# Optimization experiments

Hardware: AMD Instinct MI355X
Metric: run time of the kernel (lower is better)

## Reference

```python
import jax, jax.numpy as jnp
import numpy as np

ORIENTATIONS = 8
CELL = 16          # pixels_per_cell = (16, 16)
EPS = 1e-5         # skimage L2-Hys eps


def _hog_features(x):
    """x: [B, H, W, C] float image. Faithful to skimage.feature.hog with
    orientations=8, pixels_per_cell=(16,16), cells_per_block=(1,1),
    block_norm='L2-Hys', multichannel gradient selection."""
    B, H, W, C = x.shape
    # per-channel central-difference gradients, zero at borders (skimage _hog_channel_gradient)
    g_row = jnp.zeros_like(x).at[:, 1:-1, :, :].set(x[:, 2:, :, :] - x[:, :-2, :, :])
    g_col = jnp.zeros_like(x).at[:, :, 1:-1, :].set(x[:, :, 2:, :] - x[:, :, :-2, :])
    magn_ch = jnp.hypot(g_row, g_col)                      # [B,H,W,C]
    # pick channel with max gradient magnitude per pixel
    idx = jnp.argmax(magn_ch, axis=-1, keepdims=True)      # [B,H,W,1]
    gr = jnp.take_along_axis(g_row, idx, axis=-1)[..., 0]  # [B,H,W]
    gc = jnp.take_along_axis(g_col, idx, axis=-1)[..., 0]
    magn = jnp.take_along_axis(magn_ch, idx, axis=-1)[..., 0]
    # orientation in degrees, mod 180 (unsigned gradients)
    ori = jnp.degrees(jnp.arctan2(gr, gc)) % 180.0
    bin_width = 180.0 / ORIENTATIONS
    bin_idx = jnp.clip(jnp.floor(ori / bin_width).astype(jnp.int32), 0, ORIENTATIONS - 1)
    ncr, ncc = H // CELL, W // CELL
    # per-cell mean magnitude for each orientation bin
    hists = []
    for o in range(ORIENTATIONS):
        m = jnp.where(bin_idx == o, magn, 0.0)             # [B,H,W]
        m = m.reshape(B, ncr, CELL, ncc, CELL).mean(axis=(2, 4))  # [B,ncr,ncc]
        hists.append(m)
    hist = jnp.stack(hists, axis=-1)                       # [B,ncr,ncc,O]
    # block normalization: 1x1 cells per block, 'L2-Hys'
    n = hist / jnp.sqrt(jnp.sum(hist * hist, axis=-1, keepdims=True) + EPS ** 2)
    n = jnp.minimum(n, 0.2)
    n = n / jnp.sqrt(jnp.sum(n * n, axis=-1, keepdims=True) + EPS ** 2)
    return n.reshape(B, -1)                                # [B, ncr*ncc*O]


def setup_inputs() -> dict:
    key = jax.random.key(0)
    fake = jax.random.uniform(key, (64, 3, 512, 512), dtype=jnp.float32)
    return {"fake": fake}


def reference(fake) -> jnp.ndarray:
    x = jnp.transpose(fake, (0, 2, 3, 1))  # NCHW -> NHWC (module's permute)
    return _hog_features(x)
```

## Files before the change

### kernel.cpp

```cpp
#include <hip/hip_runtime.h>
#include <math.h>


namespace {

constexpr int Hh = 512;
constexpr int Ww = 512;
constexpr int CHN = 3;
constexpr int HW = Hh * Ww;
constexpr float TAN22 = 0.41421356237309503f;

__device__ __forceinline__ void load_row4(const float* __restrict__ xb,
                                          int h, int c0, int lane,
                                          float dst[CHN][4]) {
    const int hl = h < 0 ? 0 : (h > Hh - 1 ? Hh - 1 : h);
#pragma unroll
    for (int ch = 0; ch < CHN; ++ch) {
        const float4 v = *(const float4*)(xb + (size_t)ch * HW +
                                          (size_t)hl * Ww + c0 + (lane << 2));
        dst[ch][0] = v.x; dst[ch][1] = v.y; dst[ch][2] = v.z; dst[ch][3] = v.w;
    }
}

__global__ __launch_bounds__(256) void hog_kernel(const float* __restrict__ x,
                                                  float* __restrict__ out) {
    const int b       = blockIdx.x >> 5;
    const int cellrow = blockIdx.x & 31;
    const int tx      = threadIdx.x;
    const int lane    = tx & 63;
    const int wid     = tx >> 6;
    const int colhalf = wid & 1;
    const int strip   = wid >> 1;
    const int r0      = cellrow * 16 + strip * 8;
    const int c0      = colhalf << 8;

    const float* xb = x + (size_t)b * (CHN * HW);

    const bool bL = (colhalf == 0) & (lane == 0);
    const bool bR = (colhalf == 1) & (lane == 63);
    const int hLoff = (colhalf == 0) ? 0 : 255;
    const int hRoff = (colhalf == 0) ? 256 : 511;

    float P[CHN][4], C[CHN][4], N[CHN][4], T[CHN][4];
    load_row4(xb, r0 - 1, c0, lane, P);
    load_row4(xb, r0,     c0, lane, C);
    load_row4(xb, r0 + 1, c0, lane, N);

    float hLc[CHN], hRc[CHN], hLn[CHN], hRn[CHN];
#pragma unroll
    for (int ch = 0; ch < CHN; ++ch) {
        const float* rp = xb + (size_t)ch * HW + (size_t)r0 * Ww;
        hLc[ch] = rp[hLoff];
        hRc[ch] = rp[hRoff];
    }

    float c[8];
#pragma unroll
    for (int o = 0; o < 8; ++o) c[o] = 0.f;

#pragma unroll 1
    for (int hh = 0; hh < 8; ++hh) {
        const int h = r0 + hh;

        if (hh < 7) load_row4(xb, h + 2, c0, lane, T);
        {
            const int hn = (h + 1 > Hh - 1) ? Hh - 1 : h + 1;
#pragma unroll
            for (int ch = 0; ch < CHN; ++ch) {
                const float* rp = xb + (size_t)ch * HW + (size_t)hn * Ww;
                hLn[ch] = rp[hLoff];
                hRn[ch] = rp[hRoff];
            }
        }

        const bool rowEdge = (h == 0) | (h == Hh - 1);

        float gL[CHN], gR[CHN];
#pragma unroll
        for (int ch = 0; ch < CHN; ++ch) {
            const float su = __shfl_up(C[ch][3], 1, 64);
            const float sd = __shfl_down(C[ch][0], 1, 64);
            gL[ch] = (lane == 0)  ? hLc[ch] : su;
            gR[ch] = (lane == 63) ? hRc[ch] : sd;
        }

#pragma unroll
        for (int i = 0; i < 4; ++i) {
            float bm2 = -1.f, bgr = 0.f, bgc = 0.f;
#pragma unroll
            for (int ch = 0; ch < CHN; ++ch) {
                const float gl  = (i == 0) ? gL[ch] : C[ch][i - 1];
                const float gr_ = (i == 3) ? gR[ch] : C[ch][i + 1];
                float gcol = gr_ - gl;
                if (i == 0) gcol = bL ? 0.f : gcol;
                if (i == 3) gcol = bR ? 0.f : gcol;
                float gv = N[ch][i] - P[ch][i];
                gv = rowEdge ? 0.f : gv;
                const float m2 = fmaf(gv, gv, gcol * gcol);
                if (m2 > bm2) { bm2 = m2; bgr = gv; bgc = gcol; }
            }
            const float m = sqrtf(bm2);

            const bool flip = (bgr < 0.f) | ((bgr == 0.f) & (bgc < 0.f));
            const float bb = flip ? -bgr : bgr;
            const float A  = flip ? -bgc : bgc;
            const float Aa = fabsf(A);
            const float p1 = Aa * TAN22;
            const float p2 = bb * TAN22;
            const bool q2  = (A <= 0.f);
            const bool ge1 = (bb >= p1), ge2 = (bb >= Aa), ge3 = (p2 >= Aa);
            const bool gt1 = (bb > p1),  gt2 = (bb > Aa),  gt3 = (p2 > Aa);
            c[0] += m;
            c[1] += (q2 | ge1) ? m : 0.f;
            c[2] += (q2 | ge2) ? m : 0.f;
            c[3] += (q2 | ge3) ? m : 0.f;
            c[4] += q2 ? m : 0.f;
            c[5] += (q2 & !gt3) ? m : 0.f;
            c[6] += (q2 & !gt2) ? m : 0.f;
            c[7] += (q2 & !gt1) ? m : 0.f;
        }

        if (hh < 7) {
#pragma unroll
            for (int ch = 0; ch < CHN; ++ch) {
#pragma unroll
                for (int i = 0; i < 4; ++i) {
                    P[ch][i] = C[ch][i];
                    C[ch][i] = N[ch][i];
                    N[ch][i] = T[ch][i];
                }
                hLc[ch] = hLn[ch];
                hRc[ch] = hRn[ch];
            }
        }
    }

#pragma unroll
    for (int o = 0; o < 8; ++o) {
        c[o] += __shfl_xor(c[o], 1, 64);
        c[o] += __shfl_xor(c[o], 2, 64);
    }

    __shared__ float lh[2][32][9];
    if (tx < 64) lh[tx >> 5][tx & 31][8] = 0.f;
    if ((lane & 3) == 0) {
        const int cell = (colhalf << 4) + (lane >> 2);
#pragma unroll
        for (int o = 0; o < 8; ++o) lh[strip][cell][o] = c[o];
    }
    __syncthreads();

    const int cell = tx >> 3;
    const int o    = tx & 7;
    const float c_o  = lh[0][cell][o]     + lh[1][cell][o];
    const float c_o1 = lh[0][cell][o + 1] + lh[1][cell][o + 1];
    const float hv = (c_o - c_o1) * (1.0f / 256.0f);

    float ss = hv * hv;
    ss += __shfl_xor(ss, 1, 64);
    ss += __shfl_xor(ss, 2, 64);
    ss += __shfl_xor(ss, 4, 64);
    float n1 = hv / sqrtf(ss + 1e-10f);
    n1 = fminf(n1, 0.2f);
    float s2 = n1 * n1;
    s2 += __shfl_xor(s2, 1, 64);
    s2 += __shfl_xor(s2, 2, 64);
    s2 += __shfl_xor(s2, 4, 64);
    const float nv = n1 / sqrtf(s2 + 1e-10f);

    out[(((size_t)b * 32 + cellrow) * 32 + cell) * 8 + o] = nv;
}

}

extern "C" void kernel_launch(void* const* d_in, const int* in_sizes, int n_in,
                              void* d_out, int out_size, void* d_ws, size_t ws_size,
                              hipStream_t stream) {
    (void)n_in; (void)out_size; (void)d_ws; (void)ws_size;
    const float* x = (const float*)d_in[0];
    float* out = (float*)d_out;
    const int B = in_sizes[0] / (CHN * HW);
    const int grid = B * 32;
    hog_kernel<<<grid, 256, 0, stream>>>(x, out);
}
```

Measured before the change: 282.9 us.

## Split blocks by column half and preload all strip rows up front

Each block now covers one column half of a cell row, which doubles the grid. Each wave handles a 4-row strip instead of 8, and all six needed rows are loaded into registers before any compute starts. This replaces the rolling per-row prefetch loop, so more memory loads are in flight at once and latency is easier to hide. The horizontal halo values are fetched once per wave and handed out with shuffles instead of per-row scalar loads. In exchange, more halo rows are re-read (6 loads for 4 output rows rather than 10 for 8), register use goes up (launch bounds 256,4), and half the threads sit idle in the final normalization.

```diff
diff --git a/kernel.cpp b/kernel.cpp
--- a/kernel.cpp
+++ b/kernel.cpp
@@ -10,78 +10,59 @@
 constexpr int HW = Hh * Ww;
 constexpr float TAN22 = 0.41421356237309503f;
 
-__device__ __forceinline__ void load_row4(const float* __restrict__ xb,
-                                          int h, int c0, int lane,
-                                          float dst[CHN][4]) {
-    const int hl = h < 0 ? 0 : (h > Hh - 1 ? Hh - 1 : h);
-#pragma unroll
-    for (int ch = 0; ch < CHN; ++ch) {
-        const float4 v = *(const float4*)(xb + (size_t)ch * HW +
-                                          (size_t)hl * Ww + c0 + (lane << 2));
-        dst[ch][0] = v.x; dst[ch][1] = v.y; dst[ch][2] = v.z; dst[ch][3] = v.w;
-    }
-}
-
-__global__ __launch_bounds__(256) void hog_kernel(const float* __restrict__ x,
-                                                  float* __restrict__ out) {
-    const int b       = blockIdx.x >> 5;
-    const int cellrow = blockIdx.x & 31;
+__global__ __launch_bounds__(256, 4) void hog_kernel(const float* __restrict__ x,
+                                                     float* __restrict__ out) {
+    const int b       = blockIdx.x >> 6;
+    const int cellrow = (blockIdx.x >> 1) & 31;
+    const int colhalf = blockIdx.x & 1;
     const int tx      = threadIdx.x;
     const int lane    = tx & 63;
     const int wid     = tx >> 6;
-    const int colhalf = wid & 1;
-    const int strip   = wid >> 1;
-    const int r0      = cellrow * 16 + strip * 8;
+    const int r0      = cellrow * 16 + wid * 4;
     const int c0      = colhalf << 8;
 
     const float* xb = x + (size_t)b * (CHN * HW);
 
+    float4 R[6][CHN];
+#pragma unroll
+    for (int r = 0; r < 6; ++r) {
+        int h = r0 - 1 + r;
+        h = h < 0 ? 0 : (h > Hh - 1 ? Hh - 1 : h);
+#pragma unroll
+        for (int ch = 0; ch < CHN; ++ch)
+            R[r][ch] = *(const float4*)(xb + (size_t)ch * HW +
+                                        (size_t)h * Ww + c0 + (lane << 2));
+    }
+
+    float halov = 0.f;
+    if (lane < 24) {
+        const int ch = lane >> 3, r = (lane >> 1) & 3, side = lane & 1;
+        int wcol = side ? c0 + 256 : c0 - 1;
+        wcol = wcol < 0 ? 0 : (wcol > Ww - 1 ? Ww - 1 : wcol);
+        halov = xb[(size_t)ch * HW + (size_t)(r0 + r) * Ww + wcol];
+    }
+
     const bool bL = (colhalf == 0) & (lane == 0);
     const bool bR = (colhalf == 1) & (lane == 63);
-    const int hLoff = (colhalf == 0) ? 0 : 255;
-    const int hRoff = (colhalf == 0) ? 256 : 511;
-
-    float P[CHN][4], C[CHN][4], N[CHN][4], T[CHN][4];
-    load_row4(xb, r0 - 1, c0, lane, P);
-    load_row4(xb, r0,     c0, lane, C);
-    load_row4(xb, r0 + 1, c0, lane, N);
-
-    float hLc[CHN], hRc[CHN], hLn[CHN], hRn[CHN];
-#pragma unroll
-    for (int ch = 0; ch < CHN; ++ch) {
-        const float* rp = xb + (size_t)ch * HW + (size_t)r0 * Ww;
-        hLc[ch] = rp[hLoff];
-        hRc[ch] = rp[hRoff];
-    }
 
     float c[8];
 #pragma unroll
     for (int o = 0; o < 8; ++o) c[o] = 0.f;
 
-#pragma unroll 1
-    for (int hh = 0; hh < 8; ++hh) {
+#pragma unroll
+    for (int hh = 0; hh < 4; ++hh) {
         const int h = r0 + hh;
-
-        if (hh < 7) load_row4(xb, h + 2, c0, lane, T);
-        {
-            const int hn = (h + 1 > Hh - 1) ? Hh - 1 : h + 1;
-#pragma unroll
-            for (int ch = 0; ch < CHN; ++ch) {
-                const float* rp = xb + (size_t)ch * HW + (size_t)hn * Ww;
-                hLn[ch] = rp[hLoff];
-                hRn[ch] = rp[hRoff];
-            }
-        }
-
         const bool rowEdge = (h == 0) | (h == Hh - 1);
 
         float gL[CHN], gR[CHN];
 #pragma unroll
         for (int ch = 0; ch < CHN; ++ch) {
-            const float su = __shfl_up(C[ch][3], 1, 64);
-            const float sd = __shfl_down(C[ch][0], 1, 64);
-            gL[ch] = (lane == 0)  ? hLc[ch] : su;
-            gR[ch] = (lane == 63) ? hRc[ch] : sd;
+            const float su = __shfl_up(R[hh + 1][ch].w, 1, 64);
+            const float sd = __shfl_down(R[hh + 1][ch].x, 1, 64);
+            const float hl = __shfl(halov, (ch << 3) | (hh << 1), 64);
+            const float hr = __shfl(halov, (ch << 3) | (hh << 1) | 1, 64);
+            gL[ch] = (lane == 0)  ? hl : su;
+            gR[ch] = (lane == 63) ? hr : sd;
         }
 
 #pragma unroll
@@ -89,12 +70,18 @@
             float bm2 = -1.f, bgr = 0.f, bgc = 0.f;
 #pragma unroll
             for (int ch = 0; ch < CHN; ++ch) {
-                const float gl  = (i == 0) ? gL[ch] : C[ch][i - 1];
-                const float gr_ = (i == 3) ? gR[ch] : C[ch][i + 1];
+                const float4 pv = R[hh][ch];
+                const float4 cv = R[hh + 1][ch];
+                const float4 nv = R[hh + 2][ch];
+                const float pr_[4] = {pv.x, pv.y, pv.z, pv.w};
+                const float cu_[4] = {cv.x, cv.y, cv.z, cv.w};
+                const float nx_[4] = {nv.x, nv.y, nv.z, nv.w};
+                const float gl  = (i == 0) ? gL[ch] : cu_[i - 1];
+                const float gr_ = (i == 3) ? gR[ch] : cu_[i + 1];
                 float gcol = gr_ - gl;
                 if (i == 0) gcol = bL ? 0.f : gcol;
                 if (i == 3) gcol = bR ? 0.f : gcol;
-                float gv = N[ch][i] - P[ch][i];
+                float gv = nx_[i] - pr_[i];
                 gv = rowEdge ? 0.f : gv;
                 const float m2 = fmaf(gv, gv, gcol * gcol);
                 if (m2 > bm2) { bm2 = m2; bgr = gv; bgc = gcol; }
@@ -119,20 +106,6 @@
             c[6] += (q2 & !gt2) ? m : 0.f;
             c[7] += (q2 & !gt1) ? m : 0.f;
         }
-
-        if (hh < 7) {
-#pragma unroll
-            for (int ch = 0; ch < CHN; ++ch) {
-#pragma unroll
-                for (int i = 0; i < 4; ++i) {
-                    P[ch][i] = C[ch][i];
-                    C[ch][i] = N[ch][i];
-                    N[ch][i] = T[ch][i];
-                }
-                hLc[ch] = hLn[ch];
-                hRc[ch] = hRn[ch];
-            }
-        }
     }
 
 #pragma unroll
@@ -141,34 +114,38 @@
         c[o] += __shfl_xor(c[o], 2, 64);
     }
 
-    __shared__ float lh[2][32][9];
-    if (tx < 64) lh[tx >> 5][tx & 31][8] = 0.f;
+    __shared__ float lh[4][16][9];
+    if (tx < 64) lh[tx >> 4][tx & 15][8] = 0.f;
     if ((lane & 3) == 0) {
-        const int cell = (colhalf << 4) + (lane >> 2);
+        const int cell = lane >> 2;
 #pragma unroll
-        for (int o = 0; o < 8; ++o) lh[strip][cell][o] = c[o];
+        for (int o = 0; o < 8; ++o) lh[wid][cell][o] = c[o];
     }
     __syncthreads();
 
-    const int cell = tx >> 3;
-    const int o    = tx & 7;
-    const float c_o  = lh[0][cell][o]     + lh[1][cell][o];
-    const float c_o1 = lh[0][cell][o + 1] + lh[1][cell][o + 1];
-    const float hv = (c_o - c_o1) * (1.0f / 256.0f);
+    if (tx < 128) {
+        const int cell = tx >> 3;
+        const int o    = tx & 7;
+        const float c_o  = lh[0][cell][o]     + lh[1][cell][o] +
+                           lh[2][cell][o]     + lh[3][cell][o];
+        const float c_o1 = lh[0][cell][o + 1] + lh[1][cell][o + 1] +
+                           lh[2][cell][o + 1] + lh[3][cell][o + 1];
+        const float hv = (c_o - c_o1) * (1.0f / 256.0f);
 
-    float ss = hv * hv;
-    ss += __shfl_xor(ss, 1, 64);
-    ss += __shfl_xor(ss, 2, 64);
-    ss += __shfl_xor(ss, 4, 64);
-    float n1 = hv / sqrtf(ss + 1e-10f);
-    n1 = fminf(n1, 0.2f);
-    float s2 = n1 * n1;
-    s2 += __shfl_xor(s2, 1, 64);
-    s2 += __shfl_xor(s2, 2, 64);
-    s2 += __shfl_xor(s2, 4, 64);
-    const float nv = n1 / sqrtf(s2 + 1e-10f);
+        float ss = hv * hv;
+        ss += __shfl_xor(ss, 1, 64);
+        ss += __shfl_xor(ss, 2, 64);
+        ss += __shfl_xor(ss, 4, 64);
+        float n1 = hv / sqrtf(ss + 1e-10f);
+        n1 = fminf(n1, 0.2f);
+        float s2 = n1 * n1;
+        s2 += __shfl_xor(s2, 1, 64);
+        s2 += __shfl_xor(s2, 2, 64);
+        s2 += __shfl_xor(s2, 4, 64);
+        const float nv = n1 / sqrtf(s2 + 1e-10f);
 
-    out[(((size_t)b * 32 + cellrow) * 32 + cell) * 8 + o] = nv;
+        out[(((size_t)b * 32 + cellrow) * 32 + (colhalf * 16 + cell)) * 8 + o] = nv;
+    }
 }
 
 }
@@ -180,6 +157,6 @@
     const float* x = (const float*)d_in[0];
     float* out = (float*)d_out;
     const int B = in_sizes[0] / (CHN * HW);
-    const int grid = B * 32;
+    const int grid = B * 32 * 2;
     hog_kernel<<<grid, 256, 0, stream>>>(x, out);
 }
```

Measured after the change: 269.1 us. -4.9%, faster.
